# Optimization experiments

Measured on AMD Instinct MI355X. Metric: run time of the kernel, lower is better.

Reference implementation:

```python
import jax, jax.numpy as jnp
import numpy as np

NUM_HEADS = 12
QUERY_SCALE = 0.125  # hard-coded 1/sqrt(64) in the original module


def setup_inputs() -> dict:
    key = jax.random.key(0)
    ks = jax.random.split(key, 5)
    S, B, H = 1024, 8, 768
    return {
        "hidden_states": jax.random.normal(ks[0], (S, B, H), dtype=jnp.float32),
        "in_proj_weight": jax.random.normal(ks[1], (3 * H, H), dtype=jnp.float32) * 0.02,
        "in_proj_bias": jax.random.normal(ks[2], (3 * H,), dtype=jnp.float32) * 0.02,
        "out_proj_weight": jax.random.normal(ks[3], (H, H), dtype=jnp.float32) * 0.02,
        "out_proj_bias": jax.random.normal(ks[4], (H,), dtype=jnp.float32) * 0.02,
    }


def reference(hidden_states, in_proj_weight, in_proj_bias, out_proj_weight, out_proj_bias):
    S, B, H = hidden_states.shape
    h = NUM_HEADS
    d = H // h

    # fused QKV in-projection: (S, B, 3H)
    mixed = hidden_states @ in_proj_weight.T + in_proj_bias
    q, k, v = jnp.split(mixed, 3, axis=-1)
    q = q * QUERY_SCALE

    def to_heads(x):  # (S, B, H) -> (B*h, S, d)
        return x.reshape(S, B * h, d).transpose(1, 0, 2)

    q, k, v = to_heads(q), to_heads(k), to_heads(v)

    scores = jnp.einsum("nsd,ntd->nst", q, k)          # (B*h, S, S)
    probs = jax.nn.softmax(scores, axis=-1)            # dropout is identity in eval
    ctx = jnp.einsum("nst,ntd->nsd", probs, v)         # (B*h, S, d)

    ctx = ctx.transpose(1, 0, 2).reshape(S, B, H)      # back to (S, B, H)
    return ctx @ out_proj_weight.T + out_proj_bias
```

## Files before the change

### kernel.cpp

```cpp
#include <hip/hip_runtime.h>

#define NH 12

typedef __bf16 bf16x8 __attribute__((ext_vector_type(8)));
typedef __bf16 bf16x4 __attribute__((ext_vector_type(4)));
typedef float f32x4 __attribute__((ext_vector_type(4)));

typedef const __attribute__((address_space(1))) void* gas_ptr;
typedef __attribute__((address_space(3))) void* las_ptr;

__device__ __forceinline__ void gload_lds16(const __bf16* g, __bf16* l) {
    __builtin_amdgcn_global_load_lds((gas_ptr)g, (las_ptr)l, 16, 0, 0);
}

#define QSCALE 0.18033688011112042f

__global__ void convert_kernel(const float* __restrict__ hs,
                               const float* __restrict__ w1,
                               const float* __restrict__ w2,
                               __bf16* __restrict__ xh,
                               __bf16* __restrict__ wq,
                               __bf16* __restrict__ wo) {
    const long long C0 = 786432;
    const long long C1 = 221184;
    const long long C2 = 73728;
    long long i = (long long)blockIdx.x * blockDim.x + threadIdx.x;
    const long long stride = (long long)gridDim.x * blockDim.x;
    for (; i < C0 + C1 + C2; i += stride) {
        const float* src; __bf16* dst; long long j;
        if (i < C0)           { src = hs; dst = xh; j = i; }
        else if (i < C0 + C1) { src = w1; dst = wq; j = i - C0; }
        else                  { src = w2; dst = wo; j = i - C0 - C1; }
        f32x4 v0 = *(const f32x4*)(src + j * 8);
        f32x4 v1 = *(const f32x4*)(src + j * 8 + 4);
        bf16x8 o;
#pragma unroll
        for (int r = 0; r < 4; r++) { o[r] = (__bf16)v0[r]; o[4 + r] = (__bf16)v1[r]; }
        *(bf16x8*)(dst + j * 8) = o;
    }
}

template <int MODE>
__global__ __launch_bounds__(512) void gemm_nt(
    const __bf16* __restrict__ A, const __bf16* __restrict__ Bm,
    const float* __restrict__ bias,
    __bf16* __restrict__ qb, __bf16* __restrict__ kb, __bf16* __restrict__ vT,
    float* __restrict__ outf, int M, int N, int K, int NXB)
{
    __shared__ __bf16 As[2][128 * 64];
    __shared__ __bf16 Bs[2][128 * 64];
    const int t = threadIdx.x;
    const int lane = t & 63;
    const int w = t >> 6;
    const int wr = w >> 2, wc = w & 3;
    const int fr = lane & 15, g4 = lane >> 4;

    const int cpx = gridDim.x >> 3;
    const int orig = blockIdx.x;
    const int swz = (orig & 7) * cpx + (orig >> 3);
    const int bx = swz % NXB, by = swz / NXB;
    const int m0 = by * 128, n0 = bx * 128;

    f32x4 acc[4][2];
    const f32x4 z4 = {0.f, 0.f, 0.f, 0.f};
#pragma unroll
    for (int i = 0; i < 4; i++)
#pragma unroll
        for (int j = 0; j < 2; j++) acc[i][j] = z4;

    const int kSteps = K >> 6;

#pragma unroll
    for (int i = 0; i < 2; i++) {
        const int c = i * 512 + t;
        const int row = c >> 3;
        const int cb = ((c & 7) ^ (row & 7)) * 8;
        gload_lds16(A  + (size_t)(m0 + row) * K + cb, &As[0][c * 8]);
        gload_lds16(Bm + (size_t)(n0 + row) * K + cb, &Bs[0][c * 8]);
    }
    __syncthreads();

    int cur = 0;
    for (int ks = 0; ks < kSteps; ks++) {
        if (ks < kSteps - 1) {
            const int kt = (ks + 1) << 6;
#pragma unroll
            for (int i = 0; i < 2; i++) {
                const int c = i * 512 + t;
                const int row = c >> 3;
                const int cb = ((c & 7) ^ (row & 7)) * 8;
                gload_lds16(A  + (size_t)(m0 + row) * K + kt + cb, &As[cur ^ 1][c * 8]);
                gload_lds16(Bm + (size_t)(n0 + row) * K + kt + cb, &Bs[cur ^ 1][c * 8]);
            }
        }

#pragma unroll
        for (int h = 0; h < 2; h++) {
            bf16x8 af[4], bfr[2];
#pragma unroll
            for (int i = 0; i < 4; i++) {
                const int r = wr * 64 + i * 16 + fr;
                af[i] = *(const bf16x8*)&As[cur][r * 64 + (((h * 4 + g4) ^ (r & 7)) * 8)];
            }
#pragma unroll
            for (int j = 0; j < 2; j++) {
                const int r = wc * 32 + j * 16 + fr;
                bfr[j] = *(const bf16x8*)&Bs[cur][r * 64 + (((h * 4 + g4) ^ (r & 7)) * 8)];
            }
            __builtin_amdgcn_s_setprio(1);
#pragma unroll
            for (int i = 0; i < 4; i++)
#pragma unroll
                for (int j = 0; j < 2; j++)
                    acc[i][j] = __builtin_amdgcn_mfma_f32_16x16x32_bf16(af[i], bfr[j], acc[i][j], 0, 0, 0);
            __builtin_amdgcn_s_setprio(0);
        }
        __syncthreads();
        cur ^= 1;
    }

#pragma unroll
    for (int j = 0; j < 2; j++) {
        const int gc = n0 + wc * 32 + j * 16 + fr;
        const float bv = bias[gc];
        int which = 0, head = 0, dim = 0;
        if (MODE == 0) {
            which = gc / 768;
            const int jj = gc - which * 768;
            head = jj >> 6; dim = jj & 63;
        }
#pragma unroll
        for (int i = 0; i < 4; i++)
#pragma unroll
            for (int r = 0; r < 4; r++) {
                const int gr = m0 + wr * 64 + i * 16 + g4 * 4 + r;
                const float val = acc[i][j][r] + bv;
                if (MODE == 0) {
                    const int s = gr >> 3, b = gr & 7;
                    const size_t n = (size_t)(b * NH + head);
                    if (which == 0)      qb[(n * 1024 + s) * 64 + dim] = (__bf16)(val * QSCALE);
                    else if (which == 1) kb[(n * 1024 + s) * 64 + dim] = (__bf16)val;
                    else                 vT[(n * 64 + dim) * 1024 + s] = (__bf16)val;
                } else {
                    outf[(size_t)gr * N + gc] = val;
                }
            }
    }
}

__global__ __launch_bounds__(512) void attn_kernel(
    const __bf16* __restrict__ qb, const __bf16* __restrict__ kb,
    const __bf16* __restrict__ vT, __bf16* __restrict__ ctx)
{
    __shared__ __bf16 Kl[2][64 * 64];
    __shared__ __bf16 Vl[2][64 * 64];
    __shared__ __bf16 Pl[8][16 * 64];
    const int t = threadIdx.x, lane = t & 63, w = t >> 6;

    const int orig = blockIdx.x;
    const int swz = (orig & 7) * 96 + (orig >> 3);
    const int n = swz >> 3;
    const int q0 = (swz & 7) * 128;
    const int fr = lane & 15, g4 = lane >> 4;
    const int fx = fr & 7;

    const __bf16* qptr = qb + ((size_t)n * 1024 + q0 + w * 16 + fr) * 64 + g4 * 8;
    const bf16x8 qf0 = *(const bf16x8*)qptr;
    const bf16x8 qf1 = *(const bf16x8*)(qptr + 32);

    float mval = -1e30f, lval = 0.f;
    const f32x4 z4 = {0.f, 0.f, 0.f, 0.f};
    f32x4 o[4] = {z4, z4, z4, z4};

    const int srow = t >> 3;
    const int scb  = (t & 7) ^ (srow & 7);
    const __bf16* kbase = kb + (size_t)n * 65536;
    const __bf16* vbase = vT + (size_t)n * 65536;

    gload_lds16(kbase + (size_t)srow * 64 + scb * 8,   &Kl[0][t * 8]);
    gload_lds16(vbase + (size_t)srow * 1024 + scb * 8, &Vl[0][t * 8]);
    __syncthreads();

    int cur = 0;
    for (int kc = 0; kc < 16; kc++) {
        if (kc < 15) {
            const int t0 = (kc + 1) * 64;
            gload_lds16(kbase + (size_t)(t0 + srow) * 64 + scb * 8,  &Kl[cur ^ 1][t * 8]);
            gload_lds16(vbase + (size_t)srow * 1024 + t0 + scb * 8,  &Vl[cur ^ 1][t * 8]);
        }

        f32x4 sc[4];
        __builtin_amdgcn_s_setprio(1);
#pragma unroll
        for (int tt = 0; tt < 4; tt++) {
            const int row = (tt * 16 + fr) * 64;
            bf16x8 kf0 = *(const bf16x8*)&Kl[cur][row + ((g4 ^ fx) * 8)];
            bf16x8 kf1 = *(const bf16x8*)&Kl[cur][row + (((4 + g4) ^ fx) * 8)];
            f32x4 s = __builtin_amdgcn_mfma_f32_16x16x32_bf16(kf0, qf0, z4, 0, 0, 0);
            s = __builtin_amdgcn_mfma_f32_16x16x32_bf16(kf1, qf1, s, 0, 0, 0);
            sc[tt] = s;
        }
        __builtin_amdgcn_s_setprio(0);

        float a[16];
#pragma unroll
        for (int tt = 0; tt < 4; tt++)
#pragma unroll
            for (int r = 0; r < 4; r++) a[tt * 4 + r] = sc[tt][r];

        float m8[8];
#pragma unroll
        for (int i = 0; i < 8; i++) m8[i] = fmaxf(a[i], a[i + 8]);
        float m4a = fmaxf(m8[0], m8[4]), m4b = fmaxf(m8[1], m8[5]);
        float m4c = fmaxf(m8[2], m8[6]), m4d = fmaxf(m8[3], m8[7]);
        float pmax = fmaxf(fmaxf(m4a, m4b), fmaxf(m4c, m4d));
        pmax = fmaxf(pmax, __shfl_xor(pmax, 16));
        pmax = fmaxf(pmax, __shfl_xor(pmax, 32));

        if (pmax > mval + 8.0f) {
            const float sf = __builtin_amdgcn_exp2f(mval - pmax);
            lval *= sf;
#pragma unroll
            for (int dt = 0; dt < 4; dt++) o[dt] *= sf;
            mval = pmax;
        }

        float p[16];
#pragma unroll
        for (int i = 0; i < 16; i++) p[i] = __builtin_amdgcn_exp2f(a[i] - mval);
        float s8[8];
#pragma unroll
        for (int i = 0; i < 8; i++) s8[i] = p[i] + p[i + 8];
        float s4a = s8[0] + s8[4], s4b = s8[1] + s8[5];
        float s4c = s8[2] + s8[6], s4d = s8[3] + s8[7];
        float psum = (s4a + s4b) + (s4c + s4d);
        psum += __shfl_xor(psum, 16);
        psum += __shfl_xor(psum, 32);
        lval += psum;

#pragma unroll
        for (int tt = 0; tt < 4; tt++) {
            bf16x4 pk;
            pk[0] = (__bf16)p[tt * 4 + 0];
            pk[1] = (__bf16)p[tt * 4 + 1];
            pk[2] = (__bf16)p[tt * 4 + 2];
            pk[3] = (__bf16)p[tt * 4 + 3];
            const int blk = (2 * tt + (g4 >> 1)) ^ fx;
            *(bf16x4*)&Pl[w][fr * 64 + blk * 8 + (g4 & 1) * 4] = pk;
        }

        __builtin_amdgcn_s_setprio(1);
#pragma unroll
        for (int ks = 0; ks < 2; ks++) {
            bf16x8 pa = *(const bf16x8*)&Pl[w][fr * 64 + (((4 * ks + g4) ^ fx) * 8)];
#pragma unroll
            for (int dt = 0; dt < 4; dt++) {
                bf16x8 vf = *(const bf16x8*)&Vl[cur][(dt * 16 + fr) * 64 + (((4 * ks + g4) ^ fx) * 8)];
                o[dt] = __builtin_amdgcn_mfma_f32_16x16x32_bf16(vf, pa, o[dt], 0, 0, 0);
            }
        }
        __builtin_amdgcn_s_setprio(0);

        if (kc < 15) __syncthreads();
        cur ^= 1;
    }

    const int b = n / NH, head = n % NH;
    const float rl = 1.0f / lval;
    const int srw = q0 + w * 16 + fr;
    __bf16* cbase = ctx + ((size_t)srw * 8 + b) * 768 + head * 64;
#pragma unroll
    for (int dt = 0; dt < 4; dt++) {
        bf16x4 ov;
#pragma unroll
        for (int r = 0; r < 4; r++) ov[r] = (__bf16)(o[dt][r] * rl);
        *(bf16x4*)&cbase[dt * 16 + g4 * 4] = ov;
    }
}

extern "C" void kernel_launch(void* const* d_in, const int* in_sizes, int n_in,
                              void* d_out, int out_size, void* d_ws, size_t ws_size,
                              hipStream_t stream) {
    const float* hs = (const float*)d_in[0];
    const float* w1 = (const float*)d_in[1];
    const float* b1 = (const float*)d_in[2];
    const float* w2 = (const float*)d_in[3];
    const float* b2 = (const float*)d_in[4];
    float* out = (float*)d_out;

    char* ws = (char*)d_ws;
    __bf16* qb  = (__bf16*)(ws);
    __bf16* kb  = (__bf16*)(ws + 12582912);
    __bf16* vT  = (__bf16*)(ws + 25165824);
    __bf16* Xh  = (__bf16*)(ws + 37748736);
    __bf16* Wq  = (__bf16*)(ws + 50331648);
    __bf16* Wo  = (__bf16*)(ws + 53870592);
    __bf16* Ctx = Xh;

    convert_kernel<<<2048, 256, 0, stream>>>(hs, w1, w2, Xh, Wq, Wo);
    gemm_nt<0><<<1152, 512, 0, stream>>>(Xh, Wq, b1, qb, kb, vT, nullptr, 8192, 2304, 768, 18);
    attn_kernel<<<768, 512, 0, stream>>>(qb, kb, vT, Ctx);
    gemm_nt<1><<<384, 512, 0, stream>>>(Ctx, Wo, b2, nullptr, nullptr, nullptr, out, 8192, 768, 768, 6);
}
```

Measured before the change: 128.6 us.

## Use four-stage LDS prefetch pipeline with vmcnt waits in QKV GEMM

```diff
diff --git a/kernel.cpp b/kernel.cpp
--- a/kernel.cpp
+++ b/kernel.cpp
@@ -40,15 +40,15 @@
     }
 }
 
-template <int MODE>
+template <int MODE, int NBUF>
 __global__ __launch_bounds__(512) void gemm_nt(
     const __bf16* __restrict__ A, const __bf16* __restrict__ Bm,
     const float* __restrict__ bias,
     __bf16* __restrict__ qb, __bf16* __restrict__ kb, __bf16* __restrict__ vT,
     float* __restrict__ outf, int M, int N, int K, int NXB)
 {
-    __shared__ __bf16 As[2][128 * 64];
-    __shared__ __bf16 Bs[2][128 * 64];
+    __shared__ __bf16 As[NBUF][128 * 64];
+    __shared__ __bf16 Bs[NBUF][128 * 64];
     const int t = threadIdx.x;
     const int lane = t & 63;
     const int w = t >> 6;
@@ -70,30 +70,18 @@
 
     const int kSteps = K >> 6;
 
-#pragma unroll
-    for (int i = 0; i < 2; i++) {
-        const int c = i * 512 + t;
-        const int row = c >> 3;
-        const int cb = ((c & 7) ^ (row & 7)) * 8;
-        gload_lds16(A  + (size_t)(m0 + row) * K + cb, &As[0][c * 8]);
-        gload_lds16(Bm + (size_t)(n0 + row) * K + cb, &Bs[0][c * 8]);
-    }
-    __syncthreads();
-
-    int cur = 0;
-    for (int ks = 0; ks < kSteps; ks++) {
-        if (ks < kSteps - 1) {
-            const int kt = (ks + 1) << 6;
-#pragma unroll
-            for (int i = 0; i < 2; i++) {
-                const int c = i * 512 + t;
-                const int row = c >> 3;
-                const int cb = ((c & 7) ^ (row & 7)) * 8;
-                gload_lds16(A  + (size_t)(m0 + row) * K + kt + cb, &As[cur ^ 1][c * 8]);
-                gload_lds16(Bm + (size_t)(n0 + row) * K + kt + cb, &Bs[cur ^ 1][c * 8]);
-            }
-        }
-
+    auto stage = [&](int tk, int b) {
+#pragma unroll
+        for (int i = 0; i < 2; i++) {
+            const int c = i * 512 + t;
+            const int row = c >> 3;
+            const int cb = ((c & 7) ^ (row & 7)) * 8;
+            gload_lds16(A  + (size_t)(m0 + row) * K + tk * 64 + cb, &As[b][c * 8]);
+            gload_lds16(Bm + (size_t)(n0 + row) * K + tk * 64 + cb, &Bs[b][c * 8]);
+        }
+    };
+
+    auto compute = [&](int cur) {
 #pragma unroll
         for (int h = 0; h < 2; h++) {
             bf16x8 af[4], bfr[2];
@@ -115,8 +103,42 @@
                     acc[i][j] = __builtin_amdgcn_mfma_f32_16x16x32_bf16(af[i], bfr[j], acc[i][j], 0, 0, 0);
             __builtin_amdgcn_s_setprio(0);
         }
+    };
+
+    if constexpr (NBUF == 4) {
+        stage(0, 0);
+        if (kSteps > 1) stage(1, 1);
+        if (kSteps > 2) stage(2, 2);
+        if (kSteps > 2) asm volatile("s_waitcnt vmcnt(8)" ::: "memory");
+        else            asm volatile("s_waitcnt vmcnt(0)" ::: "memory");
+        __builtin_amdgcn_s_barrier();
+        __builtin_amdgcn_sched_barrier(0);
+
+        for (int ks = 0; ks < kSteps; ks++) {
+            const int cur = ks & 3;
+            if (ks + 3 < kSteps) stage(ks + 3, (ks + 3) & 3);
+
+            compute(cur);
+
+            const int rem = kSteps - 1 - ks;
+            if (rem >= 3)      asm volatile("s_waitcnt vmcnt(8)" ::: "memory");
+            else if (rem == 2) asm volatile("s_waitcnt vmcnt(4)" ::: "memory");
+            else if (rem == 1) asm volatile("s_waitcnt vmcnt(0)" ::: "memory");
+            if (rem >= 1) {
+                __builtin_amdgcn_s_barrier();
+                __builtin_amdgcn_sched_barrier(0);
+            }
+        }
+    } else {
+        stage(0, 0);
         __syncthreads();
-        cur ^= 1;
+        int cur = 0;
+        for (int ks = 0; ks < kSteps; ks++) {
+            if (ks < kSteps - 1) stage(ks + 1, cur ^ 1);
+            compute(cur);
+            __syncthreads();
+            cur ^= 1;
+        }
     }
 
 #pragma unroll
@@ -298,7 +320,7 @@
     __bf16* Ctx = Xh;
 
     convert_kernel<<<2048, 256, 0, stream>>>(hs, w1, w2, Xh, Wq, Wo);
-    gemm_nt<0><<<1152, 512, 0, stream>>>(Xh, Wq, b1, qb, kb, vT, nullptr, 8192, 2304, 768, 18);
+    gemm_nt<0, 4><<<1152, 512, 0, stream>>>(Xh, Wq, b1, qb, kb, vT, nullptr, 8192, 2304, 768, 18);
     attn_kernel<<<768, 512, 0, stream>>>(qb, kb, vT, Ctx);
-    gemm_nt<1><<<384, 512, 0, stream>>>(Ctx, Wo, b2, nullptr, nullptr, nullptr, out, 8192, 768, 768, 6);
-}
+    gemm_nt<1, 2><<<384, 512, 0, stream>>>(Ctx, Wo, b2, nullptr, nullptr, nullptr, out, 8192, 768, 768, 6);
+}
```

Result: slower. 148.2 us (+15.3%).

## Stage V tiles through LDS for coalesced transposed stores; shrink out-proj M tile

Applied to the files above, without the earlier changes.

```diff
diff --git a/kernel.cpp b/kernel.cpp
--- a/kernel.cpp
+++ b/kernel.cpp
@@ -40,15 +40,20 @@
     }
 }
 
-template <int MODE>
-__global__ __launch_bounds__(512) void gemm_nt(
+template <int MODE, int BM>
+__global__ __launch_bounds__(BM * 4) void gemm_nt(
     const __bf16* __restrict__ A, const __bf16* __restrict__ Bm,
     const float* __restrict__ bias,
     __bf16* __restrict__ qb, __bf16* __restrict__ kb, __bf16* __restrict__ vT,
     float* __restrict__ outf, int M, int N, int K, int NXB)
 {
-    __shared__ __bf16 As[2][128 * 64];
-    __shared__ __bf16 Bs[2][128 * 64];
+    constexpr int THREADS = BM * 4;
+    constexpr int ASZ = BM * 64 * 2;
+    constexpr int BSZ = 128 * 64 * 2;
+    constexpr int BUNITS = 1024 / THREADS;
+    constexpr int SMEMSZ = (MODE == 0) ? 66560 : (2 * ASZ + 2 * BSZ);
+    __shared__ __align__(16) char SMEM[SMEMSZ];
+
     const int t = threadIdx.x;
     const int lane = t & 63;
     const int w = t >> 6;
@@ -59,7 +64,7 @@
     const int orig = blockIdx.x;
     const int swz = (orig & 7) * cpx + (orig >> 3);
     const int bx = swz % NXB, by = swz / NXB;
-    const int m0 = by * 128, n0 = bx * 128;
+    const int m0 = by * BM, n0 = bx * 128;
 
     f32x4 acc[4][2];
     const f32x4 z4 = {0.f, 0.f, 0.f, 0.f};
@@ -70,42 +75,39 @@
 
     const int kSteps = K >> 6;
 
-#pragma unroll
-    for (int i = 0; i < 2; i++) {
-        const int c = i * 512 + t;
-        const int row = c >> 3;
-        const int cb = ((c & 7) ^ (row & 7)) * 8;
-        gload_lds16(A  + (size_t)(m0 + row) * K + cb, &As[0][c * 8]);
-        gload_lds16(Bm + (size_t)(n0 + row) * K + cb, &Bs[0][c * 8]);
-    }
-    __syncthreads();
-
-    int cur = 0;
-    for (int ks = 0; ks < kSteps; ks++) {
-        if (ks < kSteps - 1) {
-            const int kt = (ks + 1) << 6;
-#pragma unroll
-            for (int i = 0; i < 2; i++) {
-                const int c = i * 512 + t;
-                const int row = c >> 3;
-                const int cb = ((c & 7) ^ (row & 7)) * 8;
-                gload_lds16(A  + (size_t)(m0 + row) * K + kt + cb, &As[cur ^ 1][c * 8]);
-                gload_lds16(Bm + (size_t)(n0 + row) * K + kt + cb, &Bs[cur ^ 1][c * 8]);
-            }
-        }
-
+    auto As_ = [&](int b) { return (__bf16*)(SMEM + b * ASZ); };
+    auto Bs_ = [&](int b) { return (__bf16*)(SMEM + 2 * ASZ + b * BSZ); };
+
+    auto stage = [&](int tk, int b) {
+#pragma unroll
+        for (int u = 0; u < 2; u++) {
+            const int c = u * THREADS + t;
+            const int row = c >> 3;
+            const int cb = ((c & 7) ^ (row & 7)) * 8;
+            gload_lds16(A + (size_t)(m0 + row) * K + tk * 64 + cb, As_(b) + c * 8);
+        }
+#pragma unroll
+        for (int u = 0; u < BUNITS; u++) {
+            const int c = u * THREADS + t;
+            const int row = c >> 3;
+            const int cb = ((c & 7) ^ (row & 7)) * 8;
+            gload_lds16(Bm + (size_t)(n0 + row) * K + tk * 64 + cb, Bs_(b) + c * 8);
+        }
+    };
+
+    auto compute = [&](int cur) {
 #pragma unroll
         for (int h = 0; h < 2; h++) {
             bf16x8 af[4], bfr[2];
 #pragma unroll
             for (int i = 0; i < 4; i++) {
                 const int r = wr * 64 + i * 16 + fr;
-                af[i] = *(const bf16x8*)&As[cur][r * 64 + (((h * 4 + g4) ^ (r & 7)) * 8)];
+                af[i] = *(const bf16x8*)&As_(cur)[r * 64 + (((h * 4 + g4) ^ (r & 7)) * 8)];
             }
 #pragma unroll
             for (int j = 0; j < 2; j++) {
                 const int r = wc * 32 + j * 16 + fr;
-                bfr[j] = *(const bf16x8*)&Bs[cur][r * 64 + (((h * 4 + g4) ^ (r & 7)) * 8)];
+                bfr[j] = *(const bf16x8*)&Bs_(cur)[r * 64 + (((h * 4 + g4) ^ (r & 7)) * 8)];
             }
             __builtin_amdgcn_s_setprio(1);
 #pragma unroll
@@ -115,36 +117,88 @@
                     acc[i][j] = __builtin_amdgcn_mfma_f32_16x16x32_bf16(af[i], bfr[j], acc[i][j], 0, 0, 0);
             __builtin_amdgcn_s_setprio(0);
         }
+    };
+
+    stage(0, 0);
+    __syncthreads();
+    int cur = 0;
+    for (int ks = 0; ks < kSteps; ks++) {
+        if (ks < kSteps - 1) stage(ks + 1, cur ^ 1);
+        compute(cur);
         __syncthreads();
         cur ^= 1;
     }
 
-#pragma unroll
-    for (int j = 0; j < 2; j++) {
-        const int gc = n0 + wc * 32 + j * 16 + fr;
-        const float bv = bias[gc];
-        int which = 0, head = 0, dim = 0;
-        if (MODE == 0) {
-            which = gc / 768;
-            const int jj = gc - which * 768;
-            head = jj >> 6; dim = jj & 63;
-        }
-#pragma unroll
-        for (int i = 0; i < 4; i++)
-#pragma unroll
-            for (int r = 0; r < 4; r++) {
-                const int gr = m0 + wr * 64 + i * 16 + g4 * 4 + r;
-                const float val = acc[i][j][r] + bv;
-                if (MODE == 0) {
-                    const int s = gr >> 3, b = gr & 7;
-                    const size_t n = (size_t)(b * NH + head);
-                    if (which == 0)      qb[(n * 1024 + s) * 64 + dim] = (__bf16)(val * QSCALE);
-                    else if (which == 1) kb[(n * 1024 + s) * 64 + dim] = (__bf16)val;
-                    else                 vT[(n * 64 + dim) * 1024 + s] = (__bf16)val;
-                } else {
-                    outf[(size_t)gr * N + gc] = val;
+    if constexpr (MODE == 1) {
+#pragma unroll
+        for (int j = 0; j < 2; j++) {
+            const int gc = n0 + wc * 32 + j * 16 + fr;
+            const float bv = bias[gc];
+#pragma unroll
+            for (int i = 0; i < 4; i++)
+#pragma unroll
+                for (int r = 0; r < 4; r++) {
+                    const int gr = m0 + wr * 64 + i * 16 + g4 * 4 + r;
+                    outf[(size_t)gr * N + gc] = acc[i][j][r] + bv;
                 }
-            }
+        }
+    } else {
+        const int which = (n0 >= 1536) ? 2 : (n0 >= 768 ? 1 : 0);
+        if (which < 2) {
+#pragma unroll
+            for (int j = 0; j < 2; j++) {
+                const int gc = n0 + wc * 32 + j * 16 + fr;
+                const float bv = bias[gc];
+                const int jj = gc - which * 768;
+                const int head = jj >> 6, dim = jj & 63;
+#pragma unroll
+                for (int i = 0; i < 4; i++)
+#pragma unroll
+                    for (int r = 0; r < 4; r++) {
+                        const int gr = m0 + wr * 64 + i * 16 + g4 * 4 + r;
+                        const int s = gr >> 3, b = gr & 7;
+                        const size_t n = (size_t)(b * NH + head);
+                        const float val = acc[i][j][r] + bv;
+                        if (which == 0) qb[(n * 1024 + s) * 64 + dim] = (__bf16)(val * QSCALE);
+                        else            kb[(n * 1024 + s) * 64 + dim] = (__bf16)val;
+                    }
+            }
+        } else {
+            float* Cw = (float*)SMEM;
+#pragma unroll
+            for (int j = 0; j < 2; j++) {
+                const int col = wc * 32 + j * 16 + fr;
+                const float bv = bias[n0 + col];
+#pragma unroll
+                for (int i = 0; i < 4; i++)
+#pragma unroll
+                    for (int r = 0; r < 4; r++) {
+                        const int l = wr * 64 + i * 16 + g4 * 4 + r;
+                        Cw[l * 130 + col] = acc[i][j][r] + bv;
+                    }
+            }
+            __syncthreads();
+            const int hbase = (n0 - 1536) >> 6;
+            const int s0 = m0 >> 3;
+#pragma unroll
+            for (int u = 0; u < 2; u++) {
+                const int c = u * THREADS + t;
+                const int b = c >> 7;
+                const int hd = (c >> 6) & 1;
+                const int dim = c & 63;
+                const size_t n = (size_t)(b * NH + hbase + hd);
+                __bf16* dst = vT + (n * 64 + dim) * 1024 + s0;
+                bf16x8 o0, o1;
+#pragma unroll
+                for (int sl = 0; sl < 8; sl++)
+                    o0[sl] = (__bf16)Cw[(sl * 8 + b) * 130 + hd * 64 + dim];
+#pragma unroll
+                for (int sl = 0; sl < 8; sl++)
+                    o1[sl] = (__bf16)Cw[((sl + 8) * 8 + b) * 130 + hd * 64 + dim];
+                *(bf16x8*)dst = o0;
+                *(bf16x8*)(dst + 8) = o1;
+            }
+        }
     }
 }
 
@@ -298,7 +352,7 @@
     __bf16* Ctx = Xh;
 
     convert_kernel<<<2048, 256, 0, stream>>>(hs, w1, w2, Xh, Wq, Wo);
-    gemm_nt<0><<<1152, 512, 0, stream>>>(Xh, Wq, b1, qb, kb, vT, nullptr, 8192, 2304, 768, 18);
+    gemm_nt<0, 128><<<1152, 512, 0, stream>>>(Xh, Wq, b1, qb, kb, vT, nullptr, 8192, 2304, 768, 18);
     attn_kernel<<<768, 512, 0, stream>>>(qb, kb, vT, Ctx);
-    gemm_nt<1><<<384, 512, 0, stream>>>(Ctx, Wo, b2, nullptr, nullptr, nullptr, out, 8192, 768, 768, 6);
-}
+    gemm_nt<1, 64><<<768, 256, 0, stream>>>(Ctx, Wo, b2, nullptr, nullptr, nullptr, out, 8192, 768, 768, 6);
+}
```

After: 116.9 us. 9.0% less time.
